# Kernel optimization log

Hardware: AMD Instinct MI355X
Metric: run time of the kernel (lower is better)

The kernel has to match this reference:

```python
import jax, jax.numpy as jnp
import numpy as np

N_NODES = 50000
N_EDGES = 600000
IN_DIM = 128
H_DIM = 128
OUT_DIM = 128
N_REL = 8
N_BASES = 8
N_GRAPHS = 256


def _lin(key, i, o):
    return jax.random.normal(key, (i, o), dtype=jnp.float32) / np.sqrt(i)


def setup_inputs() -> dict:
    key = jax.random.key(0)
    ks = jax.random.split(key, 16)
    inp = {}
    inp["features"] = jax.random.normal(ks[0], (N_NODES, IN_DIM), dtype=jnp.float32)
    inp["src"] = jax.random.randint(ks[1], (N_EDGES,), 0, N_NODES, dtype=jnp.int32)
    inp["dst"] = jax.random.randint(ks[2], (N_EDGES,), 0, N_NODES, dtype=jnp.int32)
    inp["etype"] = jax.random.randint(ks[3], (N_EDGES,), 0, N_REL, dtype=jnp.int32)
    inp["node2graph"] = jnp.sort(jax.random.randint(ks[4], (N_NODES,), 0, N_GRAPHS, dtype=jnp.int32))
    # RelGraphConv basis-decomposed weights: bases [B,in,out], comp [R,B], bias [out]
    inp["bases1"] = jax.random.normal(ks[5], (N_BASES, IN_DIM, H_DIM), dtype=jnp.float32) / np.sqrt(IN_DIM)
    inp["comp1"] = jax.random.normal(ks[6], (N_REL, N_BASES), dtype=jnp.float32) / np.sqrt(N_BASES)
    inp["bias1"] = jnp.zeros((H_DIM,), dtype=jnp.float32)
    inp["bases2"] = jax.random.normal(ks[7], (N_BASES, H_DIM, H_DIM), dtype=jnp.float32) / np.sqrt(H_DIM)
    inp["comp2"] = jax.random.normal(ks[8], (N_REL, N_BASES), dtype=jnp.float32) / np.sqrt(N_BASES)
    inp["bias2"] = jnp.zeros((H_DIM,), dtype=jnp.float32)
    inp["bases3"] = jax.random.normal(ks[9], (N_BASES, H_DIM, OUT_DIM), dtype=jnp.float32) / np.sqrt(H_DIM)
    inp["comp3"] = jax.random.normal(ks[10], (N_REL, N_BASES), dtype=jnp.float32) / np.sqrt(N_BASES)
    inp["bias3"] = jnp.zeros((OUT_DIM,), dtype=jnp.float32)
    # attention gate + MLP head
    inp["gate_w"] = _lin(ks[11], OUT_DIM, 1)
    inp["gate_b"] = jnp.zeros((1,), dtype=jnp.float32)
    inp["fc1_w"] = _lin(ks[12], OUT_DIM, 100)
    inp["fc1_b"] = jnp.zeros((100,), dtype=jnp.float32)
    inp["fc2_w"] = _lin(ks[13], 100, 64)
    inp["fc2_b"] = jnp.zeros((64,), dtype=jnp.float32)
    inp["fc3_w"] = _lin(ks[14], 64, 1)
    inp["fc3_b"] = jnp.zeros((1,), dtype=jnp.float32)
    return inp


def _rgcn_layer(x, bases, comp, bias, src, dst, etype):
    # basis decomposition: W_r = sum_b comp[r,b] * bases[b]
    W = jnp.einsum('rb,bio->rio', comp, bases)            # [R, in, out]
    h_all = jnp.einsum('ni,rio->nro', x, W)               # [N, R, out]
    msg = h_all[src, etype]                               # gather per-edge: W_{etype} x_src, [E, out]
    agg = jax.ops.segment_sum(msg, dst, num_segments=x.shape[0])
    return agg + bias


def _segment_softmax(gate, seg, num_segments):
    # gate: [N, 1]; softmax per graph segment
    m = jax.ops.segment_max(gate, seg, num_segments=num_segments)
    e = jnp.exp(gate - m[seg])
    s = jax.ops.segment_sum(e, seg, num_segments=num_segments)
    return e / s[seg]


def reference(features, bases1, comp1, bias1, bases2, comp2, bias2,
              bases3, comp3, bias3, gate_w, gate_b,
              fc1_w, fc1_b, fc2_w, fc2_b, fc3_w, fc3_b,
              src, dst, etype, node2graph):
    h = _rgcn_layer(features, bases1, comp1, bias1, src, dst, etype)
    h = jax.nn.relu(h)  # dropout=0.0 -> identity
    h = _rgcn_layer(h, bases2, comp2, bias2, src, dst, etype)
    h = jax.nn.relu(h)
    h = _rgcn_layer(h, bases3, comp3, bias3, src, dst, etype)
    # GlobalAttentionPooling
    gate = h @ gate_w + gate_b                            # [N, 1]
    gate = _segment_softmax(gate, node2graph, N_GRAPHS)
    readout = jax.ops.segment_sum(h * gate, node2graph, num_segments=N_GRAPHS)  # [G, out]
    # MLP classifier + sigmoid
    z = jax.nn.relu(readout @ fc1_w + fc1_b)
    z = jax.nn.relu(z @ fc2_w + fc2_b)
    z = z @ fc3_w + fc3_b
    return jax.nn.sigmoid(z).squeeze(-1)                  # [G]
```

## Files before the change

### kernel.cpp

```cpp
#include <hip/hip_runtime.h>
#include <hip/hip_bf16.h>
#include <math.h>

#define N_NODES 50000
#define N_EDGES 600000
#define DIM 128
#define N_REL 8
#define N_GRAPHS 256
#define NBN 32
#define NBLK ((N_NODES + NBN - 1) / NBN)
#define KDIM (N_REL * DIM)
#define NKEY (N_NODES * N_REL)
#define SEG 1024
#define NSEG2 391

typedef __attribute__((ext_vector_type(8))) short short8;
typedef __attribute__((ext_vector_type(4))) float floatx4;
typedef __attribute__((ext_vector_type(4))) float f32x4;
typedef unsigned int uint;
typedef unsigned short ushort;

static __device__ __forceinline__ int lower_bound_i(const int* a, int n, int v) {
    int lo = 0, hi = n;
    while (lo < hi) { int mid = (lo + hi) >> 1; if (a[mid] < v) lo = mid + 1; else hi = mid; }
    return lo;
}

static __device__ __forceinline__ uint2 split2(float x, float y) {
    uint ux = __float_as_uint(x);
    uint hx = (ux + 0x7FFFu + ((ux >> 16) & 1u)) & 0xFFFF0000u;
    float rx = x - __uint_as_float(hx);
    uint urx = __float_as_uint(rx);
    uint lx = (urx + 0x7FFFu + ((urx >> 16) & 1u)) >> 16;
    uint uy = __float_as_uint(y);
    uint hy = (uy + 0x7FFFu + ((uy >> 16) & 1u)) & 0xFFFF0000u;
    float ry = y - __uint_as_float(hy);
    uint ury = __float_as_uint(ry);
    uint ly = (ury + 0x7FFFu + ((ury >> 16) & 1u)) >> 16;
    return make_uint2((hx >> 16) | (hy & 0xFFFF0000u), lx | (ly << 16));
}

__global__ void k_count(const int* __restrict__ dst, const int* __restrict__ etype,
                        int* __restrict__ counts, int e) {
    int i = blockIdx.x * blockDim.x + threadIdx.x;
    if (i < e) atomicAdd(&counts[dst[i] * 8 + etype[i]], 1);
}

__global__ __launch_bounds__(256) void k_scan_seg(const int* __restrict__ counts,
                                                  int* __restrict__ segscan,
                                                  int* __restrict__ segtot) {
    const int b = blockIdx.x, t = threadIdx.x;
    const int base = b * SEG + t * 4;
    const int4 v = *(const int4*)(counts + base);
    const int s0 = v.x, s1 = s0 + v.y, s2 = s1 + v.z, s3 = s2 + v.w;
    __shared__ int sl[256];
    sl[t] = s3;
    __syncthreads();
    for (int off = 1; off < 256; off <<= 1) {
        int add = (t >= off) ? sl[t - off] : 0;
        __syncthreads();
        sl[t] += add;
        __syncthreads();
    }
    const int tp = sl[t] - s3;
    int4 o;
    o.x = tp; o.y = tp + s0; o.z = tp + s1; o.w = tp + s2;
    *(int4*)(segscan + base) = o;
    if (t == 255) segtot[b] = sl[255];
}

__global__ __launch_bounds__(512) void k_scan_tot(const int* __restrict__ segtot,
                                                  int* __restrict__ segbase) {
    const int t = threadIdx.x;
    const int v = (t < NSEG2) ? segtot[t] : 0;
    __shared__ int sl[512];
    sl[t] = v;
    __syncthreads();
    for (int off = 1; off < 512; off <<= 1) {
        int u = (t >= off) ? sl[t - off] : 0;
        __syncthreads();
        sl[t] += u;
        __syncthreads();
    }
    if (t < NSEG2) segbase[t] = sl[t] - v;
    if (t == NSEG2) segbase[NSEG2] = sl[NSEG2 - 1];
}

__global__ void k_scan_fin(const int* __restrict__ segscan, const int* __restrict__ segbase,
                           int* __restrict__ offsets, int* __restrict__ cursor) {
    const int i = blockIdx.x * blockDim.x + threadIdx.x;
    if (i < NKEY) {
        const int val = segbase[i >> 10] + segscan[i];
        offsets[i] = val;
        cursor[i] = val;
    } else if (i == NKEY) {
        offsets[NKEY] = segbase[NSEG2];
    }
}

__global__ void k_fill(const int* __restrict__ src, const int* __restrict__ dst,
                       const int* __restrict__ etype, int* cursor,
                       int* __restrict__ edges, int e) {
    int i = blockIdx.x * blockDim.x + threadIdx.x;
    if (i < e) {
        const int et = etype[i];
        int pos = atomicAdd(&cursor[dst[i] * 8 + et], 1);
        edges[pos] = src[i] | (et << 16);
    }
}

__global__ void k_packW3(const float* __restrict__ b1, const float* __restrict__ c1,
                         ushort* __restrict__ Whi1, ushort* __restrict__ Wlo1,
                         const float* __restrict__ b2, const float* __restrict__ c2,
                         ushort* __restrict__ Whi2, ushort* __restrict__ Wlo2,
                         const float* __restrict__ b3, const float* __restrict__ c3,
                         ushort* __restrict__ Whi3, ushort* __restrict__ Wlo3) {
    const int lay = blockIdx.x >> 9;
    const int id = (blockIdx.x & 511) * blockDim.x + threadIdx.x;
    const float* bases = (lay == 0) ? b1 : (lay == 1) ? b2 : b3;
    const float* comp  = (lay == 0) ? c1 : (lay == 1) ? c2 : c3;
    ushort* Whi = (lay == 0) ? Whi1 : (lay == 1) ? Whi2 : Whi3;
    ushort* Wlo = (lay == 0) ? Wlo1 : (lay == 1) ? Wlo2 : Wlo3;
    int nn = id & 127, k = id >> 7;
    int r = k >> 7, dk = k & 127;
    const float* cp = comp + r * 8;
    float v = 0.f;
#pragma unroll
    for (int b = 0; b < 8; b++) v = fmaf(cp[b], bases[((size_t)b * 128 + dk) * 128 + nn], v);
    uint u = __float_as_uint(v);
    uint hu = (u + 0x7FFFu + ((u >> 16) & 1u)) & 0xFFFF0000u;
    float rf = v - __uint_as_float(hu);
    uint ur = __float_as_uint(rf);
    uint lu = (ur + 0x7FFFu + ((ur >> 16) & 1u)) >> 16;
    int kt = k >> 5, kk = k & 31;
    int off = kt * 4096 + nn * 32 + kk;
    Whi[off] = (ushort)(hu >> 16);
    Wlo[off] = (ushort)lu;
}

template <bool RELU, bool GATE>
__global__ __launch_bounds__(512, 8) void k_layer(
    const float* __restrict__ xin, float* __restrict__ hout,
    const int* __restrict__ edges, const int* __restrict__ offsets,
    const ushort* __restrict__ Whi, const ushort* __restrict__ Wlo,
    const float* __restrict__ bias,
    const float* __restrict__ gw, const float* __restrict__ gb,
    float* __restrict__ gate) {
    __shared__ ushort sHi[8 * 1024];
    __shared__ ushort sLo[8 * 1024];
    __shared__ float sgatep[NBN][8];
    const int tid = threadIdx.x;
    const int lane = tid & 63;
    const int w = tid >> 6;
    const int q2 = lane >> 4, mm = lane & 15;
    const int xev = (mm ^ q2) * 8;
    const int xod = ((mm ^ q2) ^ 4) * 8;
    const int aq = q2 * 256;
    const int n0 = w * 16 + mm;
    const ushort* bph = Whi + n0 * 32 + q2 * 8;
    const ushort* bpl = Wlo + n0 * 32 + q2 * 8;
    floatx4 acc0 = {0.f, 0.f, 0.f, 0.f};
    floatx4 acc1 = {0.f, 0.f, 0.f, 0.f};

    const int hw = tid >> 5, l5 = tid & 31;
    const int d0 = l5 * 4;
    const int kt_off = l5 >> 3;
    const int q = (l5 >> 1) & 3;
    const int jb = (l5 & 1) * 4;

    for (int ro = 0; ro < 4; ++ro) {
        for (int v = 0; v < 2; ++v) {
            const int m = hw * 2 + v;
            const int n = blockIdx.x * NBN + m;
            int e = 0, e1 = 0;
            if (n < N_NODES) { e = offsets[n * 8 + ro * 2]; e1 = offsets[n * 8 + ro * 2 + 2]; }
            f32x4 a0 = (f32x4)0.f, a1 = (f32x4)0.f;
            while (e < e1) {
                const int c = e1 - e;
                const int p0 = edges[e];
                const int p1 = (c > 1) ? edges[e + 1] : 0;
                const int p2 = (c > 2) ? edges[e + 2] : 0;
                const int p3 = (c > 3) ? edges[e + 3] : 0;
                f32x4 v0, v1, v2, v3;
                v0 = *(const f32x4*)(xin + (size_t)(p0 & 0xFFFF) * DIM + d0);
                if (c > 1) v1 = *(const f32x4*)(xin + (size_t)(p1 & 0xFFFF) * DIM + d0);
                if (c > 2) v2 = *(const f32x4*)(xin + (size_t)(p2 & 0xFFFF) * DIM + d0);
                if (c > 3) v3 = *(const f32x4*)(xin + (size_t)(p3 & 0xFFFF) * DIM + d0);
                if (p0 & 0x10000) a1 += v0; else a0 += v0;
                if (c > 1) { if (p1 & 0x10000) a1 += v1; else a0 += v1; }
                if (c > 2) { if (p2 & 0x10000) a1 += v2; else a0 += v2; }
                if (c > 3) { if (p3 & 0x10000) a1 += v3; else a0 += v3; }
                e += 4;
            }
            {
                const int ktp0 = kt_off;
                const int ch0 = q * 32 + ((m ^ q) ^ ((ktp0 & 1) << 2));
                const int u0 = ktp0 * 1024 + ch0 * 8 + jb;
                const uint2 h01 = split2(a0.x, a0.y);
                const uint2 h23 = split2(a0.z, a0.w);
                *(uint2*)(sHi + u0) = make_uint2(h01.x, h23.x);
                *(uint2*)(sLo + u0) = make_uint2(h01.y, h23.y);
                const int ktp1 = 4 + kt_off;
                const int ch1 = q * 32 + ((m ^ q) ^ ((ktp1 & 1) << 2));
                const int u1 = ktp1 * 1024 + ch1 * 8 + jb;
                const uint2 g01 = split2(a1.x, a1.y);
                const uint2 g23 = split2(a1.z, a1.w);
                *(uint2*)(sHi + u1) = make_uint2(g01.x, g23.x);
                *(uint2*)(sLo + u1) = make_uint2(g01.y, g23.y);
            }
        }
        __syncthreads();

        for (int kt = 0; kt < 8; kt += 2) {
            {
                const int ktg = ro * 8 + kt;
                const ushort* ap = sHi + kt * 1024 + aq;
                const ushort* alp = sLo + kt * 1024 + aq;
                const short8 ah0 = *(const short8*)(ap + xev);
                const short8 ah1 = *(const short8*)(ap + 128 + xev);
                const short8 al0 = *(const short8*)(alp + xev);
                const short8 al1 = *(const short8*)(alp + 128 + xev);
                const short8 bh = *(const short8*)(bph + ktg * 4096);
                const short8 bl = *(const short8*)(bpl + ktg * 4096);
                acc0 = __builtin_amdgcn_mfma_f32_16x16x32_bf16(ah0, bh, acc0, 0, 0, 0);
                acc1 = __builtin_amdgcn_mfma_f32_16x16x32_bf16(ah1, bh, acc1, 0, 0, 0);
                acc0 = __builtin_amdgcn_mfma_f32_16x16x32_bf16(ah0, bl, acc0, 0, 0, 0);
                acc1 = __builtin_amdgcn_mfma_f32_16x16x32_bf16(ah1, bl, acc1, 0, 0, 0);
                acc0 = __builtin_amdgcn_mfma_f32_16x16x32_bf16(al0, bh, acc0, 0, 0, 0);
                acc1 = __builtin_amdgcn_mfma_f32_16x16x32_bf16(al1, bh, acc1, 0, 0, 0);
            }
            {
                const int kto = kt + 1;
                const int ktg = ro * 8 + kto;
                const ushort* ap = sHi + kto * 1024 + aq;
                const ushort* alp = sLo + kto * 1024 + aq;
                const short8 ah0 = *(const short8*)(ap + xod);
                const short8 ah1 = *(const short8*)(ap + 128 + xod);
                const short8 al0 = *(const short8*)(alp + xod);
                const short8 al1 = *(const short8*)(alp + 128 + xod);
                const short8 bh = *(const short8*)(bph + ktg * 4096);
                const short8 bl = *(const short8*)(bpl + ktg * 4096);
                acc0 = __builtin_amdgcn_mfma_f32_16x16x32_bf16(ah0, bh, acc0, 0, 0, 0);
                acc1 = __builtin_amdgcn_mfma_f32_16x16x32_bf16(ah1, bh, acc1, 0, 0, 0);
                acc0 = __builtin_amdgcn_mfma_f32_16x16x32_bf16(ah0, bl, acc0, 0, 0, 0);
                acc1 = __builtin_amdgcn_mfma_f32_16x16x32_bf16(ah1, bl, acc1, 0, 0, 0);
                acc0 = __builtin_amdgcn_mfma_f32_16x16x32_bf16(al0, bh, acc0, 0, 0, 0);
                acc1 = __builtin_amdgcn_mfma_f32_16x16x32_bf16(al1, bh, acc1, 0, 0, 0);
            }
        }
        if (ro < 3) __syncthreads();
    }

    const float b0 = bias[n0];
    float gp0[4], gp1[4];
#pragma unroll
    for (int r = 0; r < 4; r++) {
        const int row0 = q2 * 4 + r;
        const int nodeA = blockIdx.x * NBN + row0;
        const int nodeB = nodeA + 16;
        float v0 = acc0[r] + b0;
        float v1 = acc1[r] + b0;
        if (RELU) { v0 = fmaxf(v0, 0.f); v1 = fmaxf(v1, 0.f); }
        if (nodeA < N_NODES) hout[(size_t)nodeA * DIM + n0] = v0;
        if (nodeB < N_NODES) hout[(size_t)nodeB * DIM + n0] = v1;
        if (GATE) { gp0[r] = v0 * gw[n0]; gp1[r] = v1 * gw[n0]; }
    }
    if (GATE) {
#pragma unroll
        for (int r = 0; r < 4; r++) {
#pragma unroll
            for (int s = 1; s < 16; s <<= 1) {
                gp0[r] += __shfl_xor(gp0[r], s, 16);
                gp1[r] += __shfl_xor(gp1[r], s, 16);
            }
        }
        __syncthreads();
        if (mm == 0) {
#pragma unroll
            for (int r = 0; r < 4; r++) {
                sgatep[q2 * 4 + r][w] = gp0[r];
                sgatep[16 + q2 * 4 + r][w] = gp1[r];
            }
        }
        __syncthreads();
        if (tid < NBN) {
            const int n = blockIdx.x * NBN + tid;
            if (n < N_NODES) {
                float s = 0.f;
#pragma unroll
                for (int w8 = 0; w8 < 8; w8++) s += sgatep[tid][w8];
                gate[n] = s + gb[0];
            }
        }
    }
}

__global__ __launch_bounds__(256) void k_pool(
    const float* __restrict__ h3, const float* __restrict__ gate, const int* __restrict__ n2g,
    const float* __restrict__ fc1w, const float* __restrict__ fc1b,
    const float* __restrict__ fc2w, const float* __restrict__ fc2b,
    const float* __restrict__ fc3w, const float* __restrict__ fc3b,
    float* __restrict__ out, int N) {
    const int g = blockIdx.x;
    const int tid = threadIdx.x;
    __shared__ float sred[256];
    __shared__ float sr[128];
    __shared__ float sz1[100];
    __shared__ float sz2[64];
    __shared__ float sm, ssum;

    const int s = lower_bound_i(n2g, N, g);
    const int e = lower_bound_i(n2g, N, g + 1);

    float m = -3.4e38f;
    for (int n = s + tid; n < e; n += 256) m = fmaxf(m, gate[n]);
    sred[tid] = m;
    __syncthreads();
    for (int off = 128; off > 0; off >>= 1) {
        if (tid < off) sred[tid] = fmaxf(sred[tid], sred[tid + off]);
        __syncthreads();
    }
    if (tid == 0) sm = sred[0];
    __syncthreads();
    const float mm = sm;

    float sum = 0.f;
    for (int n = s + tid; n < e; n += 256) sum += expf(gate[n] - mm);
    sred[tid] = sum;
    __syncthreads();
    for (int off = 128; off > 0; off >>= 1) {
        if (tid < off) sred[tid] += sred[tid + off];
        __syncthreads();
    }
    if (tid == 0) ssum = sred[0];
    __syncthreads();
    const float inv = (e > s) ? 1.0f / ssum : 0.f;

    const int col = tid & 127;
    const int half = tid >> 7;
    float acc = 0.f;
    int n = s + half;
    for (; n + 6 < e; n += 8) {
        const float w0 = expf(gate[n] - mm);
        const float w1 = expf(gate[n + 2] - mm);
        const float w2 = expf(gate[n + 4] - mm);
        const float w3 = expf(gate[n + 6] - mm);
        const float a0 = h3[(size_t)n * DIM + col];
        const float a1 = h3[(size_t)(n + 2) * DIM + col];
        const float a2 = h3[(size_t)(n + 4) * DIM + col];
        const float a3 = h3[(size_t)(n + 6) * DIM + col];
        acc = fmaf(w0, a0, acc);
        acc = fmaf(w1, a1, acc);
        acc = fmaf(w2, a2, acc);
        acc = fmaf(w3, a3, acc);
    }
    for (; n < e; n += 2) {
        const float wgt = expf(gate[n] - mm);
        acc = fmaf(wgt, h3[(size_t)n * DIM + col], acc);
    }
    sred[tid] = acc;
    __syncthreads();
    if (tid < 128) sr[tid] = (sred[tid] + sred[tid + 128]) * inv;
    __syncthreads();

    if (tid < 100) {
        float t = fc1b[tid];
        for (int i = 0; i < 128; i++) t = fmaf(sr[i], fc1w[i * 100 + tid], t);
        sz1[tid] = fmaxf(t, 0.f);
    }
    __syncthreads();
    if (tid < 64) {
        float t = fc2b[tid];
        for (int i = 0; i < 100; i++) t = fmaf(sz1[i], fc2w[i * 64 + tid], t);
        sz2[tid] = fmaxf(t, 0.f);
    }
    __syncthreads();
    if (tid < 64) {
        float p = sz2[tid] * fc3w[tid];
#pragma unroll
        for (int off = 32; off > 0; off >>= 1) p += __shfl_down(p, off, 64);
        if (tid == 0) {
            const float z = p + fc3b[0];
            out[g] = 1.0f / (1.0f + expf(-z));
        }
    }
}

extern "C" void kernel_launch(void* const* d_in, const int* in_sizes, int n_in,
                              void* d_out, int out_size, void* d_ws, size_t ws_size,
                              hipStream_t stream) {
    (void)in_sizes; (void)n_in; (void)out_size; (void)ws_size;
    const float* features = (const float*)d_in[0];
    const int*   src      = (const int*)d_in[1];
    const int*   dst      = (const int*)d_in[2];
    const int*   etype    = (const int*)d_in[3];
    const int*   n2g      = (const int*)d_in[4];
    const float* bases1   = (const float*)d_in[5];
    const float* comp1    = (const float*)d_in[6];
    const float* bias1    = (const float*)d_in[7];
    const float* bases2   = (const float*)d_in[8];
    const float* comp2    = (const float*)d_in[9];
    const float* bias2    = (const float*)d_in[10];
    const float* bases3   = (const float*)d_in[11];
    const float* comp3    = (const float*)d_in[12];
    const float* bias3    = (const float*)d_in[13];
    const float* gate_w   = (const float*)d_in[14];
    const float* gate_b   = (const float*)d_in[15];
    const float* fc1w     = (const float*)d_in[16];
    const float* fc1b     = (const float*)d_in[17];
    const float* fc2w     = (const float*)d_in[18];
    const float* fc2b     = (const float*)d_in[19];
    const float* fc3w     = (const float*)d_in[20];
    const float* fc3b     = (const float*)d_in[21];
    float* out = (float*)d_out;

    char* w = (char*)d_ws;
    auto alloc = [&](size_t bytes) -> char* {
        char* p = w;
        w += (bytes + 255) & ~(size_t)255;
        return p;
    };
    int*    offsets = (int*)alloc((NKEY + 1) * sizeof(int));
    int*    edges   = (int*)alloc((N_EDGES + 16) * sizeof(int));
    float*  hA      = (float*)alloc((size_t)N_NODES * DIM * sizeof(float));
    float*  hB      = (float*)alloc((size_t)N_NODES * DIM * sizeof(float));
    float*  gate    = (float*)alloc(N_NODES * sizeof(float));
    ushort* Whi1    = (ushort*)alloc((size_t)KDIM * DIM * sizeof(ushort));
    ushort* Wlo1    = (ushort*)alloc((size_t)KDIM * DIM * sizeof(ushort));
    ushort* Whi2    = (ushort*)alloc((size_t)KDIM * DIM * sizeof(ushort));
    ushort* Wlo2    = (ushort*)alloc((size_t)KDIM * DIM * sizeof(ushort));
    ushort* Whi3    = (ushort*)alloc((size_t)KDIM * DIM * sizeof(ushort));
    ushort* Wlo3    = (ushort*)alloc((size_t)KDIM * DIM * sizeof(ushort));
    int*    cursor  = (int*)hB;
    int*    segscan = (int*)((char*)hB + (2u << 20));
    int*    segtot  = (int*)((char*)hB + (4u << 20));
    int*    segbase = (int*)((char*)hB + (4u << 20) + 4096);

    k_packW3<<<1536, 256, 0, stream>>>(bases1, comp1, Whi1, Wlo1,
                                       bases2, comp2, Whi2, Wlo2,
                                       bases3, comp3, Whi3, Wlo3);

    hipMemsetAsync(cursor, 0, (size_t)NSEG2 * SEG * sizeof(int), stream);
    k_count<<<(N_EDGES + 255) / 256, 256, 0, stream>>>(dst, etype, cursor, N_EDGES);
    k_scan_seg<<<NSEG2, 256, 0, stream>>>(cursor, segscan, segtot);
    k_scan_tot<<<1, 512, 0, stream>>>(segtot, segbase);
    k_scan_fin<<<(NKEY + 256) / 256, 256, 0, stream>>>(segscan, segbase, offsets, cursor);
    k_fill<<<(N_EDGES + 255) / 256, 256, 0, stream>>>(src, dst, etype, cursor, edges, N_EDGES);

    k_layer<true, false><<<NBLK, 512, 0, stream>>>(features, hA, edges, offsets, Whi1, Wlo1, bias1, gate_w, gate_b, gate);
    k_layer<true, false><<<NBLK, 512, 0, stream>>>(hA, hB, edges, offsets, Whi2, Wlo2, bias2, gate_w, gate_b, gate);
    k_layer<false, true><<<NBLK, 512, 0, stream>>>(hB, hA, edges, offsets, Whi3, Wlo3, bias3, gate_w, gate_b, gate);

    k_pool<<<N_GRAPHS, 256, 0, stream>>>(hA, gate, n2g, fc1w, fc1b, fc2w, fc2b, fc3w, fc3b, out, N_NODES);
}
```

Baseline: 460.4 us.

## Double node tile to 64, process one relation per pass with edge prefetch

Each block now handles 64 nodes with four MFMA accumulators per wave, so every weight fragment load is reused across twice as many rows. The relation loop processes one relation per pass over eight passes, prefetching the next node's edge indices and the next relation's offsets. The cursor memset is folded into the weight-packing kernel to save a launch. The risks are more register pressure, fewer blocks for load balance, and twice as many barriers per block.

```diff
diff --git a/kernel.cpp b/kernel.cpp
--- a/kernel.cpp
+++ b/kernel.cpp
@@ -7,7 +7,7 @@
 #define DIM 128
 #define N_REL 8
 #define N_GRAPHS 256
-#define NBN 32
+#define NBN 64
 #define NBLK ((N_NODES + NBN - 1) / NBN)
 #define KDIM (N_REL * DIM)
 #define NKEY (N_NODES * N_REL)
@@ -109,12 +109,18 @@
     }
 }
 
-__global__ void k_packW3(const float* __restrict__ b1, const float* __restrict__ c1,
-                         ushort* __restrict__ Whi1, ushort* __restrict__ Wlo1,
-                         const float* __restrict__ b2, const float* __restrict__ c2,
-                         ushort* __restrict__ Whi2, ushort* __restrict__ Wlo2,
-                         const float* __restrict__ b3, const float* __restrict__ c3,
-                         ushort* __restrict__ Whi3, ushort* __restrict__ Wlo3) {
+__global__ void k_prep(const float* __restrict__ b1, const float* __restrict__ c1,
+                       ushort* __restrict__ Whi1, ushort* __restrict__ Wlo1,
+                       const float* __restrict__ b2, const float* __restrict__ c2,
+                       ushort* __restrict__ Whi2, ushort* __restrict__ Wlo2,
+                       const float* __restrict__ b3, const float* __restrict__ c3,
+                       ushort* __restrict__ Whi3, ushort* __restrict__ Wlo3,
+                       int* __restrict__ counts) {
+    if (blockIdx.x >= 1536) {
+        const int i = (blockIdx.x - 1536) * 1024 + threadIdx.x * 4;
+        *(int4*)(counts + i) = make_int4(0, 0, 0, 0);
+        return;
+    }
     const int lay = blockIdx.x >> 9;
     const int id = (blockIdx.x & 511) * blockDim.x + threadIdx.x;
     const float* bases = (lay == 0) ? b1 : (lay == 1) ? b2 : b3;
@@ -146,8 +152,8 @@
     const float* __restrict__ bias,
     const float* __restrict__ gw, const float* __restrict__ gb,
     float* __restrict__ gate) {
-    __shared__ ushort sHi[8 * 1024];
-    __shared__ ushort sLo[8 * 1024];
+    __shared__ ushort sHi[4 * 2048];
+    __shared__ ushort sLo[4 * 2048];
     __shared__ float sgatep[NBN][8];
     const int tid = threadIdx.x;
     const int lane = tid & 63;
@@ -155,115 +161,158 @@
     const int q2 = lane >> 4, mm = lane & 15;
     const int xev = (mm ^ q2) * 8;
     const int xod = ((mm ^ q2) ^ 4) * 8;
-    const int aq = q2 * 256;
+    const int aq = q2 * 512;
     const int n0 = w * 16 + mm;
     const ushort* bph = Whi + n0 * 32 + q2 * 8;
     const ushort* bpl = Wlo + n0 * 32 + q2 * 8;
     floatx4 acc0 = {0.f, 0.f, 0.f, 0.f};
     floatx4 acc1 = {0.f, 0.f, 0.f, 0.f};
+    floatx4 acc2 = {0.f, 0.f, 0.f, 0.f};
+    floatx4 acc3 = {0.f, 0.f, 0.f, 0.f};
 
     const int hw = tid >> 5, l5 = tid & 31;
     const int d0 = l5 * 4;
     const int kt_off = l5 >> 3;
     const int q = (l5 >> 1) & 3;
     const int jb = (l5 & 1) * 4;
-
-    for (int ro = 0; ro < 4; ++ro) {
-        for (int v = 0; v < 2; ++v) {
-            const int m = hw * 2 + v;
-            const int n = blockIdx.x * NBN + m;
-            int e = 0, e1 = 0;
-            if (n < N_NODES) { e = offsets[n * 8 + ro * 2]; e1 = offsets[n * 8 + ro * 2 + 2]; }
-            f32x4 a0 = (f32x4)0.f, a1 = (f32x4)0.f;
+    const int nbase = blockIdx.x * NBN + hw * 4;
+
+    int eS[4], eE[4];
+#pragma unroll
+    for (int v = 0; v < 4; ++v) {
+        const int n = nbase + v;
+        if (n < N_NODES) { eS[v] = offsets[n * 8]; eE[v] = offsets[n * 8 + 1]; }
+        else { eS[v] = 0; eE[v] = 0; }
+    }
+
+    for (int ro = 0; ro < 8; ++ro) {
+        int c0 = edges[eS[0]], c1 = edges[eS[0] + 1], c2 = edges[eS[0] + 2], c3 = edges[eS[0] + 3];
+#pragma unroll
+        for (int v = 0; v < 4; ++v) {
+            int f0 = 0, f1 = 0, f2 = 0, f3 = 0;
+            if (v < 3) {
+                const int es = eS[v + 1];
+                f0 = edges[es]; f1 = edges[es + 1]; f2 = edges[es + 2]; f3 = edges[es + 3];
+            }
+            f32x4 a0 = (f32x4)0.f;
+            int e = eS[v]; const int e1 = eE[v];
+            int p0 = c0, p1 = c1, p2 = c2, p3 = c3;
             while (e < e1) {
                 const int c = e1 - e;
-                const int p0 = edges[e];
-                const int p1 = (c > 1) ? edges[e + 1] : 0;
-                const int p2 = (c > 2) ? edges[e + 2] : 0;
-                const int p3 = (c > 3) ? edges[e + 3] : 0;
                 f32x4 v0, v1, v2, v3;
                 v0 = *(const f32x4*)(xin + (size_t)(p0 & 0xFFFF) * DIM + d0);
                 if (c > 1) v1 = *(const f32x4*)(xin + (size_t)(p1 & 0xFFFF) * DIM + d0);
                 if (c > 2) v2 = *(const f32x4*)(xin + (size_t)(p2 & 0xFFFF) * DIM + d0);
                 if (c > 3) v3 = *(const f32x4*)(xin + (size_t)(p3 & 0xFFFF) * DIM + d0);
-                if (p0 & 0x10000) a1 += v0; else a0 += v0;
-                if (c > 1) { if (p1 & 0x10000) a1 += v1; else a0 += v1; }
-                if (c > 2) { if (p2 & 0x10000) a1 += v2; else a0 += v2; }
-                if (c > 3) { if (p3 & 0x10000) a1 += v3; else a0 += v3; }
+                a0 += v0;
+                if (c > 1) a0 += v1;
+                if (c > 2) a0 += v2;
+                if (c > 3) a0 += v3;
                 e += 4;
+                if (e < e1) { p0 = edges[e]; p1 = edges[e + 1]; p2 = edges[e + 2]; p3 = edges[e + 3]; }
             }
             {
-                const int ktp0 = kt_off;
-                const int ch0 = q * 32 + ((m ^ q) ^ ((ktp0 & 1) << 2));
-                const int u0 = ktp0 * 1024 + ch0 * 8 + jb;
-                const uint2 h01 = split2(a0.x, a0.y);
-                const uint2 h23 = split2(a0.z, a0.w);
-                *(uint2*)(sHi + u0) = make_uint2(h01.x, h23.x);
-                *(uint2*)(sLo + u0) = make_uint2(h01.y, h23.y);
-                const int ktp1 = 4 + kt_off;
-                const int ch1 = q * 32 + ((m ^ q) ^ ((ktp1 & 1) << 2));
-                const int u1 = ktp1 * 1024 + ch1 * 8 + jb;
-                const uint2 g01 = split2(a1.x, a1.y);
-                const uint2 g23 = split2(a1.z, a1.w);
-                *(uint2*)(sHi + u1) = make_uint2(g01.x, g23.x);
-                *(uint2*)(sLo + u1) = make_uint2(g01.y, g23.y);
-            }
-        }
-        __syncthreads();
-
-        for (int kt = 0; kt < 8; kt += 2) {
+                const int m = hw * 4 + v;
+                const int ktp = kt_off;
+                const int ch = (m ^ q) ^ ((ktp & 1) << 2);
+                const int u0 = ktp * 2048 + q * 512 + ch * 8 + jb;
+                const uint2 p01 = split2(a0.x, a0.y);
+                const uint2 p23 = split2(a0.z, a0.w);
+                *(uint2*)(sHi + u0) = make_uint2(p01.x, p23.x);
+                *(uint2*)(sLo + u0) = make_uint2(p01.y, p23.y);
+            }
+            c0 = f0; c1 = f1; c2 = f2; c3 = f3;
+        }
+        __syncthreads();
+
+        int nE[4];
+        if (ro < 7) {
+#pragma unroll
+            for (int v = 0; v < 4; ++v) {
+                const int n = nbase + v;
+                nE[v] = (n < N_NODES) ? offsets[n * 8 + ro + 2] : 0;
+            }
+        }
+
+        for (int kt = 0; kt < 4; kt += 2) {
             {
-                const int ktg = ro * 8 + kt;
-                const ushort* ap = sHi + kt * 1024 + aq;
-                const ushort* alp = sLo + kt * 1024 + aq;
+                const int ktg = ro * 4 + kt;
+                const ushort* ap = sHi + kt * 2048 + aq;
+                const ushort* alp = sLo + kt * 2048 + aq;
                 const short8 ah0 = *(const short8*)(ap + xev);
                 const short8 ah1 = *(const short8*)(ap + 128 + xev);
+                const short8 ah2 = *(const short8*)(ap + 256 + xev);
+                const short8 ah3 = *(const short8*)(ap + 384 + xev);
                 const short8 al0 = *(const short8*)(alp + xev);
                 const short8 al1 = *(const short8*)(alp + 128 + xev);
+                const short8 al2 = *(const short8*)(alp + 256 + xev);
+                const short8 al3 = *(const short8*)(alp + 384 + xev);
                 const short8 bh = *(const short8*)(bph + ktg * 4096);
                 const short8 bl = *(const short8*)(bpl + ktg * 4096);
                 acc0 = __builtin_amdgcn_mfma_f32_16x16x32_bf16(ah0, bh, acc0, 0, 0, 0);
                 acc1 = __builtin_amdgcn_mfma_f32_16x16x32_bf16(ah1, bh, acc1, 0, 0, 0);
+                acc2 = __builtin_amdgcn_mfma_f32_16x16x32_bf16(ah2, bh, acc2, 0, 0, 0);
+                acc3 = __builtin_amdgcn_mfma_f32_16x16x32_bf16(ah3, bh, acc3, 0, 0, 0);
                 acc0 = __builtin_amdgcn_mfma_f32_16x16x32_bf16(ah0, bl, acc0, 0, 0, 0);
                 acc1 = __builtin_amdgcn_mfma_f32_16x16x32_bf16(ah1, bl, acc1, 0, 0, 0);
+                acc2 = __builtin_amdgcn_mfma_f32_16x16x32_bf16(ah2, bl, acc2, 0, 0, 0);
+                acc3 = __builtin_amdgcn_mfma_f32_16x16x32_bf16(ah3, bl, acc3, 0, 0, 0);
                 acc0 = __builtin_amdgcn_mfma_f32_16x16x32_bf16(al0, bh, acc0, 0, 0, 0);
                 acc1 = __builtin_amdgcn_mfma_f32_16x16x32_bf16(al1, bh, acc1, 0, 0, 0);
+                acc2 = __builtin_amdgcn_mfma_f32_16x16x32_bf16(al2, bh, acc2, 0, 0, 0);
+                acc3 = __builtin_amdgcn_mfma_f32_16x16x32_bf16(al3, bh, acc3, 0, 0, 0);
             }
             {
                 const int kto = kt + 1;
-                const int ktg = ro * 8 + kto;
-                const ushort* ap = sHi + kto * 1024 + aq;
-                const ushort* alp = sLo + kto * 1024 + aq;
+                const int ktg = ro * 4 + kto;
+                const ushort* ap = sHi + kto * 2048 + aq;
+                const ushort* alp = sLo + kto * 2048 + aq;
                 const short8 ah0 = *(const short8*)(ap + xod);
                 const short8 ah1 = *(const short8*)(ap + 128 + xod);
+                const short8 ah2 = *(const short8*)(ap + 256 + xod);
+                const short8 ah3 = *(const short8*)(ap + 384 + xod);
                 const short8 al0 = *(const short8*)(alp + xod);
                 const short8 al1 = *(const short8*)(alp + 128 + xod);
+                const short8 al2 = *(const short8*)(alp + 256 + xod);
+                const short8 al3 = *(const short8*)(alp + 384 + xod);
                 const short8 bh = *(const short8*)(bph + ktg * 4096);
                 const short8 bl = *(const short8*)(bpl + ktg * 4096);
                 acc0 = __builtin_amdgcn_mfma_f32_16x16x32_bf16(ah0, bh, acc0, 0, 0, 0);
                 acc1 = __builtin_amdgcn_mfma_f32_16x16x32_bf16(ah1, bh, acc1, 0, 0, 0);
+                acc2 = __builtin_amdgcn_mfma_f32_16x16x32_bf16(ah2, bh, acc2, 0, 0, 0);
+                acc3 = __builtin_amdgcn_mfma_f32_16x16x32_bf16(ah3, bh, acc3, 0, 0, 0);
                 acc0 = __builtin_amdgcn_mfma_f32_16x16x32_bf16(ah0, bl, acc0, 0, 0, 0);
                 acc1 = __builtin_amdgcn_mfma_f32_16x16x32_bf16(ah1, bl, acc1, 0, 0, 0);
+                acc2 = __builtin_amdgcn_mfma_f32_16x16x32_bf16(ah2, bl, acc2, 0, 0, 0);
+                acc3 = __builtin_amdgcn_mfma_f32_16x16x32_bf16(ah3, bl, acc3, 0, 0, 0);
                 acc0 = __builtin_amdgcn_mfma_f32_16x16x32_bf16(al0, bh, acc0, 0, 0, 0);
                 acc1 = __builtin_amdgcn_mfma_f32_16x16x32_bf16(al1, bh, acc1, 0, 0, 0);
-            }
-        }
-        if (ro < 3) __syncthreads();
+                acc2 = __builtin_amdgcn_mfma_f32_16x16x32_bf16(al2, bh, acc2, 0, 0, 0);
+                acc3 = __builtin_amdgcn_mfma_f32_16x16x32_bf16(al3, bh, acc3, 0, 0, 0);
+            }
+        }
+        if (ro < 7) {
+#pragma unroll
+            for (int v = 0; v < 4; ++v) { eS[v] = eE[v]; eE[v] = nE[v]; }
+            __syncthreads();
+        }
     }
 
     const float b0 = bias[n0];
-    float gp0[4], gp1[4];
+    const float gwn = GATE ? gw[n0] : 0.f;
+    float gp0[4], gp1[4], gp2[4], gp3[4];
 #pragma unroll
     for (int r = 0; r < 4; r++) {
-        const int row0 = q2 * 4 + r;
-        const int nodeA = blockIdx.x * NBN + row0;
-        const int nodeB = nodeA + 16;
-        float v0 = acc0[r] + b0;
-        float v1 = acc1[r] + b0;
-        if (RELU) { v0 = fmaxf(v0, 0.f); v1 = fmaxf(v1, 0.f); }
-        if (nodeA < N_NODES) hout[(size_t)nodeA * DIM + n0] = v0;
-        if (nodeB < N_NODES) hout[(size_t)nodeB * DIM + n0] = v1;
-        if (GATE) { gp0[r] = v0 * gw[n0]; gp1[r] = v1 * gw[n0]; }
+        const int row = q2 * 4 + r;
+        const int nA = blockIdx.x * NBN + row;
+        const int nB = nA + 16, nC = nA + 32, nD = nA + 48;
+        float v0 = acc0[r] + b0, v1 = acc1[r] + b0, v2 = acc2[r] + b0, v3 = acc3[r] + b0;
+        if (RELU) { v0 = fmaxf(v0, 0.f); v1 = fmaxf(v1, 0.f); v2 = fmaxf(v2, 0.f); v3 = fmaxf(v3, 0.f); }
+        if (nA < N_NODES) hout[(size_t)nA * DIM + n0] = v0;
+        if (nB < N_NODES) hout[(size_t)nB * DIM + n0] = v1;
+        if (nC < N_NODES) hout[(size_t)nC * DIM + n0] = v2;
+        if (nD < N_NODES) hout[(size_t)nD * DIM + n0] = v3;
+        if (GATE) { gp0[r] = v0 * gwn; gp1[r] = v1 * gwn; gp2[r] = v2 * gwn; gp3[r] = v3 * gwn; }
     }
     if (GATE) {
 #pragma unroll
@@ -272,6 +321,8 @@
             for (int s = 1; s < 16; s <<= 1) {
                 gp0[r] += __shfl_xor(gp0[r], s, 16);
                 gp1[r] += __shfl_xor(gp1[r], s, 16);
+                gp2[r] += __shfl_xor(gp2[r], s, 16);
+                gp3[r] += __shfl_xor(gp3[r], s, 16);
             }
         }
         __syncthreads();
@@ -280,6 +331,8 @@
             for (int r = 0; r < 4; r++) {
                 sgatep[q2 * 4 + r][w] = gp0[r];
                 sgatep[16 + q2 * 4 + r][w] = gp1[r];
+                sgatep[32 + q2 * 4 + r][w] = gp2[r];
+                sgatep[48 + q2 * 4 + r][w] = gp3[r];
             }
         }
         __syncthreads();
@@ -436,11 +489,10 @@
     int*    segtot  = (int*)((char*)hB + (4u << 20));
     int*    segbase = (int*)((char*)hB + (4u << 20) + 4096);
 
-    k_packW3<<<1536, 256, 0, stream>>>(bases1, comp1, Whi1, Wlo1,
-                                       bases2, comp2, Whi2, Wlo2,
-                                       bases3, comp3, Whi3, Wlo3);
-
-    hipMemsetAsync(cursor, 0, (size_t)NSEG2 * SEG * sizeof(int), stream);
+    k_prep<<<1536 + 391, 256, 0, stream>>>(bases1, comp1, Whi1, Wlo1,
+                                           bases2, comp2, Whi2, Wlo2,
+                                           bases3, comp3, Whi3, Wlo3, cursor);
+
     k_count<<<(N_EDGES + 255) / 256, 256, 0, stream>>>(dst, etype, cursor, N_EDGES);
     k_scan_seg<<<NSEG2, 256, 0, stream>>>(cursor, segscan, segtot);
     k_scan_tot<<<1, 512, 0, stream>>>(segtot, segbase);
```

After: 828.4 us. 79.9% more time.
